# Kernel tuning notes

Hardware: AMD Instinct MI355X
Metric: run time of the kernel (lower is better)

## Reference

```python
import jax, jax.numpy as jnp
import numpy as np

EPS = 1e-9
N_HEAD = 16


def clamp_c(c):
    return jnp.clip(c, 1e-4, 1.0)


def _heads(x, H):
    B, T, C = x.shape
    return x.reshape(B, T, H, C // H)


def mobius_add(x, y, c_clamped, H):
    # per-head Mobius addition; c_clamped: (H,)
    B, T, C = x.shape
    cr = c_clamped.reshape(1, 1, H, 1)
    xr, yr = _heads(x, H), _heads(y, H)
    xn = jnp.sum(xr * xr, axis=-1, keepdims=True)
    yn = jnp.sum(yr * yr, axis=-1, keepdims=True)
    ip = jnp.sum(xr * yr, axis=-1, keepdims=True)
    num = (1 + 2 * cr * ip + cr * yn) * xr + (1 - cr * xn) * yr
    den = 1 + 2 * cr * ip + cr ** 2 * xn * yn
    return (num / (den + EPS)).reshape(B, T, C)


def expmap(x, v, c, H):
    # exponential map of tangent vector v at point x (per-head curvature)
    B, T, C = x.shape
    cc = clamp_c(c)
    cr = cc.reshape(1, 1, H, 1)
    xr, vr = _heads(x, H), _heads(v, H)
    sf = 2.0 / (1 + cr * jnp.sum(xr * xr, axis=-1, keepdims=True) + EPS)  # scaling factor
    vns = jnp.sum(vr * vr, axis=-1, keepdims=True)
    vn = jnp.sqrt(vns + EPS)
    tanh_arg = jnp.abs(cr * sf * vns / 2)
    coeff = (1.0 / (jnp.sqrt(jnp.abs(cr) + EPS) + EPS)) * jnp.tanh(jnp.sqrt(tanh_arg + EPS))
    second = (coeff * vr / (vn + EPS)).reshape(B, T, C)
    return mobius_add(x, second, cc, H)


def layernorm(x, g):
    m = jnp.mean(x, axis=-1, keepdims=True)
    v = jnp.mean((x - m) ** 2, axis=-1, keepdims=True)
    return (x - m) * jax.lax.rsqrt(v + 1e-5) * g


def attention(x, w_qkv, w_proj, H):
    B, T, C = x.shape
    hs = C // H
    q, k, v = jnp.split(x @ w_qkv.T, 3, axis=-1)
    q = q.reshape(B, T, H, hs).transpose(0, 2, 1, 3)
    k = k.reshape(B, T, H, hs).transpose(0, 2, 1, 3)
    v = v.reshape(B, T, H, hs).transpose(0, 2, 1, 3)
    att = jnp.einsum('bhqd,bhkd->bhqk', q, k) * (float(hs) ** -0.5)
    mask = jnp.tril(jnp.ones((T, T), dtype=bool))
    att = jnp.where(mask, att, -jnp.inf)
    att = jax.nn.softmax(att, axis=-1)
    y = jnp.einsum('bhqk,bhkd->bhqd', att, v)
    y = y.transpose(0, 2, 1, 3).reshape(B, T, C)
    return y @ w_proj.T


def setup_inputs() -> dict:
    key = jax.random.key(0)
    ks = jax.random.split(key, 9)
    B, T, C = 2, 2048, 1024
    s = 0.02
    return {
        'x': jax.random.normal(ks[0], (B, T, C), jnp.float32) * s,
        'ln1_g': jnp.ones((C,), jnp.float32),
        'w_qkv': jax.random.normal(ks[1], (3 * C, C), jnp.float32) * s,
        'w_attn_proj': jax.random.normal(ks[2], (C, C), jnp.float32) * s,
        'c_attn': jax.random.uniform(ks[3], (N_HEAD,), jnp.float32, 0.1, 0.9),
        'ln2_g': jnp.ones((C,), jnp.float32),
        'w_fc': jax.random.normal(ks[4], (4 * C, C), jnp.float32) * s,
        'w_mlp_proj': jax.random.normal(ks[5], (C, 4 * C), jnp.float32) * s,
        'c_mlp': jax.random.uniform(ks[6], (N_HEAD,), jnp.float32, 0.1, 0.9),
    }


def reference(x, ln1_g, w_qkv, w_attn_proj, c_attn, ln2_g, w_fc, w_mlp_proj, c_mlp):
    H = N_HEAD
    a = attention(layernorm(x, ln1_g), w_qkv, w_attn_proj, H)
    x = expmap(x, a, c_attn, H)  # hyperbolic residual (attn)
    h = jax.nn.gelu(layernorm(x, ln2_g) @ w_fc.T, approximate=False) @ w_mlp_proj.T
    x = expmap(x, h, c_mlp, H)   # hyperbolic residual (mlp)
    return x
```

## Files before the change

kernel.cpp:

```cpp
#include <hip/hip_runtime.h>
#include <hip/hip_bf16.h>

typedef __attribute__((ext_vector_type(8))) short bf16x8;
typedef __attribute__((ext_vector_type(4))) float f32x4;

typedef const __attribute__((address_space(1))) void gv_t;
typedef __attribute__((address_space(3))) void lv_t;
#define GLL16(g, l) __builtin_amdgcn_global_load_lds((gv_t*)(g), (lv_t*)(l), 16, 0, 0)

#define WAITV4()  asm volatile("s_waitcnt vmcnt(4)" ::: "memory")
#define WAITV0()  asm volatile("s_waitcnt vmcnt(0)" ::: "memory")
#define WAITL0()  asm volatile("s_waitcnt lgkmcnt(0)" ::: "memory")
#define SCHEDB()  __builtin_amdgcn_sched_barrier(0)
#define BARRAW()  __builtin_amdgcn_s_barrier()

__device__ __forceinline__ short f2bf(float f) {
    __hip_bfloat16 h = __float2bfloat16(f);
    return *reinterpret_cast<short*>(&h);
}

__device__ __forceinline__ float wred(float v) {
    #pragma unroll
    for (int m = 1; m < 64; m <<= 1) v += __shfl_xor(v, m);
    return v;
}

__global__ __launch_bounds__(256) void cvt_kernel(const float* __restrict__ in,
                                                  short* __restrict__ out, int n4) {
    int i = blockIdx.x * 256 + threadIdx.x;
    if (i < n4) {
        float4 v = ((const float4*)in)[i];
        short4 o;
        o.x = f2bf(v.x); o.y = f2bf(v.y); o.z = f2bf(v.z); o.w = f2bf(v.w);
        ((short4*)out)[i] = o;
    }
}

__global__ __launch_bounds__(256) void ln_kernel(const float* __restrict__ x,
                                                 const float* __restrict__ g,
                                                 short* __restrict__ y) {
    const int row = blockIdx.x, tid = threadIdx.x;
    const float4 v = ((const float4*)(x + (size_t)row * 1024))[tid];
    float s = v.x + v.y + v.z + v.w;
    float s2 = v.x * v.x + v.y * v.y + v.z * v.z + v.w * v.w;
    #pragma unroll
    for (int m = 1; m < 64; m <<= 1) { s += __shfl_xor(s, m); s2 += __shfl_xor(s2, m); }
    __shared__ float rs[4], rs2[4];
    if ((tid & 63) == 0) { rs[tid >> 6] = s; rs2[tid >> 6] = s2; }
    __syncthreads();
    s = rs[0] + rs[1] + rs[2] + rs[3];
    s2 = rs2[0] + rs2[1] + rs2[2] + rs2[3];
    const float mean = s * (1.0f / 1024.0f);
    const float var = s2 * (1.0f / 1024.0f) - mean * mean;
    const float r = rsqrtf(var + 1e-5f);
    const float4 gg = ((const float4*)g)[tid];
    short4 o;
    o.x = f2bf((v.x - mean) * r * gg.x);
    o.y = f2bf((v.y - mean) * r * gg.y);
    o.z = f2bf((v.z - mean) * r * gg.z);
    o.w = f2bf((v.w - mean) * r * gg.w);
    ((short4*)y)[(size_t)row * 256 + tid] = o;
}

template <int EPI>
__global__ __launch_bounds__(256, 3) void gemm_bt(const short* __restrict__ A,
                                                  const short* __restrict__ Bw,
                                                  int M, int N, int LDK, int KL,
                                                  void* __restrict__ o0,
                                                  void* __restrict__ o1,
                                                  void* __restrict__ o2) {
    __shared__ __align__(16) short As[3][128 * 32];
    __shared__ __align__(16) short Bs[3][128 * 32];
    const int tid = threadIdx.x;
    const int wid = tid >> 6, lane = tid & 63;
    const int wm = wid >> 1, wn = wid & 1;
    const int col = lane & 15, grp = lane >> 4;
    const int m0 = blockIdx.x * 128, n0 = blockIdx.y * 128;
    const int z = blockIdx.z;
    f32x4 acc[4][4] = {};
    const short* ga = A + (size_t)m0 * LDK + (size_t)z * KL;
    const short* gb = Bw + (size_t)n0 * LDK + (size_t)z * KL;

#define GSTAGE(b_, t_) do {                                                     \
        const int k0_ = (t_) * 32;                                              \
        _Pragma("unroll")                                                       \
        for (int c = 0; c < 2; ++c) {                                           \
            const int row = wid * 32 + c * 16 + (lane >> 2);                    \
            const int slot = (lane & 3) ^ ((row >> 1) & 3);                     \
            GLL16(ga + (size_t)row * LDK + k0_ + slot * 8,                      \
                  (char*)&As[b_][0] + (wid * 32 + c * 16) * 64);                \
            GLL16(gb + (size_t)row * LDK + k0_ + slot * 8,                      \
                  (char*)&Bs[b_][0] + (wid * 32 + c * 16) * 64);                \
        }                                                                       \
    } while (0)

    const int NT = KL >> 5;
    GSTAGE(0, 0);
    GSTAGE(1, 1);
    WAITV4(); SCHEDB();
    BARRAW();
    for (int t = 0; t < NT; ++t) {
        const int cur = t % 3;
        if (t + 2 < NT) GSTAGE((t + 2) % 3, t + 2);
        const char* At = (const char*)&As[cur][0];
        const char* Bt = (const char*)&Bs[cur][0];
        bf16x8 af[4], bf[4];
        #pragma unroll
        for (int i = 0; i < 4; ++i) {
            const int rowA = wm * 64 + i * 16 + col;
            const int rowB = wn * 64 + i * 16 + col;
            af[i] = *(const bf16x8*)(At + rowA * 64 + ((grp ^ ((rowA >> 1) & 3)) << 4));
            bf[i] = *(const bf16x8*)(Bt + rowB * 64 + ((grp ^ ((rowB >> 1) & 3)) << 4));
        }
        #pragma unroll
        for (int mi = 0; mi < 4; ++mi)
            #pragma unroll
            for (int ni = 0; ni < 4; ++ni)
                acc[mi][ni] = __builtin_amdgcn_mfma_f32_16x16x32_bf16(af[mi], bf[ni], acc[mi][ni], 0, 0, 0);
        if (t + 1 < NT) {
            WAITL0();
            if (t + 2 < NT) { WAITV4(); } else { WAITV0(); }
            SCHEDB();
            BARRAW();
        }
    }
#undef GSTAGE
    #pragma unroll
    for (int mi = 0; mi < 4; ++mi) {
        #pragma unroll
        for (int ni = 0; ni < 4; ++ni) {
            #pragma unroll
            for (int i = 0; i < 4; ++i) {
                const int m = m0 + wm * 64 + mi * 16 + grp * 4 + i;
                const int n = n0 + wn * 64 + ni * 16 + col;
                const float v = acc[mi][ni][i];
                if (EPI == 0) {
                    const int b = m >> 11, t = m & 2047;
                    const int which = n >> 10, nn = n & 1023;
                    const int h = nn >> 6, d = nn & 63;
                    const size_t bh = (size_t)(b * 16 + h);
                    if (which == 0)
                        ((short*)o0)[(bh * 2048 + t) * 64 + d] = f2bf(v * 0.125f);
                    else if (which == 1)
                        ((short*)o1)[(bh * 2048 + t) * 64 + d] = f2bf(v);
                    else
                        ((short*)o2)[(bh * 64 + d) * 2048 + t] = f2bf(v);
                } else if (EPI == 1) {
                    float* dst = (z == 0) ? (float*)o0 : (float*)o1;
                    dst[(size_t)m * N + n] = v;
                } else {
                    const float gl = 0.5f * v * (1.0f + erff(v * 0.70710678118654752f));
                    ((short*)o0)[(size_t)m * N + n] = f2bf(gl);
                }
            }
        }
    }
}

__global__ __launch_bounds__(256, 3) void attn_kernel(const short* __restrict__ Q,
                                                      const short* __restrict__ Kg,
                                                      const short* __restrict__ VT,
                                                      short* __restrict__ Y) {
    __shared__ __align__(16) short Ks[2][4096];
    __shared__ __align__(16) short Vs[2][4096];
    __shared__ __align__(16) short Plds[4][16 * 72];
    const int j = 31 - blockIdx.x;
    const int bh = blockIdx.y;
    const int tid = threadIdx.x, wid = tid >> 6, lane = tid & 63;
    const int ql = lane & 15, g = lane >> 4;
    const int r8 = lane >> 3, s8 = lane & 7;
    const int q0s = j * 64 + wid * 16;
    const int lt = j;
    const short* Qb = Q + (size_t)bh * 2048 * 64;
    const short* Kb = Kg + (size_t)bh * 2048 * 64;
    const short* Vb = VT + (size_t)bh * 64 * 2048;
    short* Pw = &Plds[wid][0];

    bf16x8 qf0 = *(const bf16x8*)&Qb[(size_t)(q0s + ql) * 64 + 8 * g];
    bf16x8 qf1 = *(const bf16x8*)&Qb[(size_t)(q0s + ql) * 64 + 32 + 8 * g];
    f32x4 o[4] = {};
    float m = -1e30f, lsum = 0.0f;

#define STAGE(b_, kt_) do {                                                      \
        const int kbase_ = (kt_) * 64;                                           \
        _Pragma("unroll")                                                        \
        for (int c = 0; c < 2; ++c) {                                            \
            const int row = c * 32 + wid * 8 + r8;                               \
            const int slot = s8 ^ (row & 7);                                     \
            GLL16(Kb + (size_t)(kbase_ + row) * 64 + slot * 8,                   \
                  (char*)&Ks[b_][0] + c * 4096 + wid * 1024);                    \
            GLL16(Vb + (size_t)row * 2048 + kbase_ + slot * 8,                   \
                  (char*)&Vs[b_][0] + c * 4096 + wid * 1024);                    \
        }                                                                        \
    } while (0)

    STAGE(0, 0);
    __syncthreads();
    int buf = 0;
    for (int kt = 0; kt <= lt; ++kt) {
        if (kt < lt) STAGE(buf ^ 1, kt + 1);
        const int kbase = kt * 64;
        const short* Kt = &Ks[buf][0];
        const short* Vt = &Vs[buf][0];
        bf16x8 kf[4][2];
        #pragma unroll
        for (int kb = 0; kb < 4; ++kb) {
            const int row = 16 * kb + ql;
            const int x = row & 7;
            kf[kb][0] = *(const bf16x8*)((const char*)Kt + row * 128 + ((g ^ x) << 4));
            kf[kb][1] = *(const bf16x8*)((const char*)Kt + row * 128 + (((4 + g) ^ x) << 4));
        }
        f32x4 s[4];
        #pragma unroll
        for (int kb = 0; kb < 4; ++kb) {
            f32x4 z = {0.f, 0.f, 0.f, 0.f};
            z = __builtin_amdgcn_mfma_f32_16x16x32_bf16(kf[kb][0], qf0, z, 0, 0, 0);
            z = __builtin_amdgcn_mfma_f32_16x16x32_bf16(kf[kb][1], qf1, z, 0, 0, 0);
            s[kb] = z;
        }
        if (kbase + 63 > q0s) {
            #pragma unroll
            for (int kb = 0; kb < 4; ++kb)
                #pragma unroll
                for (int r = 0; r < 4; ++r)
                    if (kbase + 16 * kb + 4 * g + r > q0s + ql) s[kb][r] = -1e30f;
        }
        float t0 = fmaxf(fmaxf(s[0][0], s[0][1]), fmaxf(s[0][2], s[0][3]));
        float t1 = fmaxf(fmaxf(s[1][0], s[1][1]), fmaxf(s[1][2], s[1][3]));
        float t2 = fmaxf(fmaxf(s[2][0], s[2][1]), fmaxf(s[2][2], s[2][3]));
        float t3 = fmaxf(fmaxf(s[3][0], s[3][1]), fmaxf(s[3][2], s[3][3]));
        float tmax = fmaxf(fmaxf(t0, t1), fmaxf(t2, t3));
        tmax = fmaxf(tmax, __shfl_xor(tmax, 16));
        tmax = fmaxf(tmax, __shfl_xor(tmax, 32));
        const float mnew = fmaxf(m, tmax);
        const float sc = __expf(m - mnew);
        m = mnew;
        float rsum = 0.0f;
        #pragma unroll
        for (int kb = 0; kb < 4; ++kb) {
            const float e0 = __expf(s[kb][0] - mnew);
            const float e1 = __expf(s[kb][1] - mnew);
            const float e2 = __expf(s[kb][2] - mnew);
            const float e3 = __expf(s[kb][3] - mnew);
            rsum += (e0 + e1) + (e2 + e3);
            short4 pk;
            pk.x = f2bf(e0); pk.y = f2bf(e1); pk.z = f2bf(e2); pk.w = f2bf(e3);
            *(short4*)&Pw[ql * 72 + 16 * kb + 4 * g] = pk;
        }
        rsum += __shfl_xor(rsum, 16);
        rsum += __shfl_xor(rsum, 32);
        lsum = lsum * sc + rsum;
        #pragma unroll
        for (int nf = 0; nf < 4; ++nf)
            #pragma unroll
            for (int r = 0; r < 4; ++r) o[nf][r] *= sc;
        const bf16x8 pb0 = *(const bf16x8*)&Pw[ql * 72 + 8 * g];
        const bf16x8 pb1 = *(const bf16x8*)&Pw[ql * 72 + 32 + 8 * g];
        #pragma unroll
        for (int nf = 0; nf < 4; ++nf) {
            const int row = 16 * nf + ql;
            const int x = row & 7;
            bf16x8 v0 = *(const bf16x8*)((const char*)Vt + row * 128 + ((g ^ x) << 4));
            bf16x8 v1 = *(const bf16x8*)((const char*)Vt + row * 128 + (((4 + g) ^ x) << 4));
            o[nf] = __builtin_amdgcn_mfma_f32_16x16x32_bf16(v0, pb0, o[nf], 0, 0, 0);
            o[nf] = __builtin_amdgcn_mfma_f32_16x16x32_bf16(v1, pb1, o[nf], 0, 0, 0);
        }
        __syncthreads();
        buf ^= 1;
    }
#undef STAGE
    const int b = bh >> 4, h = bh & 15;
    const float inv = 1.0f / lsum;
    const size_t rowoff = ((size_t)b * 2048 + q0s + ql) * 1024 + h * 64;
    #pragma unroll
    for (int nf = 0; nf < 4; ++nf) {
        short4 w;
        w.x = f2bf(o[nf][0] * inv);
        w.y = f2bf(o[nf][1] * inv);
        w.z = f2bf(o[nf][2] * inv);
        w.w = f2bf(o[nf][3] * inv);
        *(short4*)&Y[rowoff + 16 * nf + 4 * g] = w;
    }
}

__global__ __launch_bounds__(256) void expmap_kernel(const float* __restrict__ x,
                                                     const float* __restrict__ va,
                                                     const float* __restrict__ vb,
                                                     const float* __restrict__ carr,
                                                     float* __restrict__ out) {
    const int blk = blockIdx.x;
    const int row = blk >> 2;
    const int head = (blk & 3) * 4 + (threadIdx.x >> 6);
    const int lane = threadIdx.x & 63;
    const size_t idx = (size_t)row * 1024 + head * 64 + lane;
    float c = carr[head];
    c = fminf(fmaxf(c, 1e-4f), 1.0f);
    const float xe = x[idx], ve = va[idx] + vb[idx];
    const float xn = wred(xe * xe);
    const float vns = wred(ve * ve);
    const float vn = sqrtf(vns + 1e-9f);
    const float sf = 2.0f / (1.0f + c * xn + 1e-9f);
    const float targ = fabsf(0.5f * c * sf * vns);
    const float coeff = (1.0f / (sqrtf(c + 1e-9f) + 1e-9f)) * tanhf(sqrtf(targ + 1e-9f));
    const float ye = coeff * ve / (vn + 1e-9f);
    const float yn = wred(ye * ye);
    const float ip = wred(xe * ye);
    const float num = (1.0f + 2.0f * c * ip + c * yn) * xe + (1.0f - c * xn) * ye;
    const float den = 1.0f + 2.0f * c * ip + c * c * xn * yn;
    out[idx] = num / (den + 1e-9f);
}

extern "C" void kernel_launch(void* const* d_in, const int* in_sizes, int n_in,
                              void* d_out, int out_size, void* d_ws, size_t ws_size,
                              hipStream_t stream) {
    (void)in_sizes; (void)n_in; (void)out_size; (void)ws_size;
    const float* x      = (const float*)d_in[0];
    const float* ln1_g  = (const float*)d_in[1];
    const float* w_qkv  = (const float*)d_in[2];
    const float* w_proj = (const float*)d_in[3];
    const float* c_attn = (const float*)d_in[4];
    const float* ln2_g  = (const float*)d_in[5];
    const float* w_fc   = (const float*)d_in[6];
    const float* w_mlp  = (const float*)d_in[7];
    const float* c_mlp  = (const float*)d_in[8];
    float* out = (float*)d_out;
    char* ws = (char*)d_ws;
    const size_t MB = 1024 * 1024;

    short* wqkv_bf  = (short*)(ws + 0 * MB);
    short* wproj_bf = (short*)(ws + 6 * MB);
    short* wfc_bf   = (short*)(ws + 8 * MB);
    short* wmlp_bf  = (short*)(ws + 16 * MB);
    short* y_bf     = (short*)(ws + 24 * MB);
    short* q_bf     = (short*)(ws + 32 * MB);
    short* k_bf     = (short*)(ws + 40 * MB);
    short* vT_bf    = (short*)(ws + 48 * MB);
    short* att_bf   = (short*)(ws + 56 * MB);
    float* a0       = (float*)(ws + 64 * MB);
    float* a1       = (float*)(ws + 80 * MB);
    float* x1       = (float*)(ws + 40 * MB);
    short* g_bf     = (short*)(ws + 56 * MB);
    float* h0       = (float*)(ws + 0 * MB);
    float* h1       = (float*)(ws + 24 * MB);

    cvt_kernel<<<3072, 256, 0, stream>>>(w_qkv, wqkv_bf, 3072 * 1024 / 4);
    cvt_kernel<<<1024, 256, 0, stream>>>(w_proj, wproj_bf, 1024 * 1024 / 4);
    cvt_kernel<<<4096, 256, 0, stream>>>(w_fc, wfc_bf, 4096 * 1024 / 4);
    cvt_kernel<<<4096, 256, 0, stream>>>(w_mlp, wmlp_bf, 1024 * 4096 / 4);

    ln_kernel<<<4096, 256, 0, stream>>>(x, ln1_g, y_bf);
    gemm_bt<0><<<dim3(32, 24, 1), 256, 0, stream>>>(y_bf, wqkv_bf, 4096, 3072, 1024, 1024,
                                                    q_bf, k_bf, vT_bf);
    attn_kernel<<<dim3(32, 32), 256, 0, stream>>>(q_bf, k_bf, vT_bf, att_bf);
    gemm_bt<1><<<dim3(32, 8, 2), 256, 0, stream>>>(att_bf, wproj_bf, 4096, 1024, 1024, 512,
                                                   a0, a1, nullptr);
    expmap_kernel<<<16384, 256, 0, stream>>>(x, a0, a1, c_attn, x1);
    ln_kernel<<<4096, 256, 0, stream>>>(x1, ln2_g, y_bf);
    gemm_bt<2><<<dim3(32, 32, 1), 256, 0, stream>>>(y_bf, wfc_bf, 4096, 4096, 1024, 1024,
                                                    g_bf, nullptr, nullptr);
    gemm_bt<1><<<dim3(32, 8, 2), 256, 0, stream>>>(g_bf, wmlp_bf, 4096, 1024, 4096, 2048,
                                                   h0, h1, nullptr);
    expmap_kernel<<<16384, 256, 0, stream>>>(x1, h0, h1, c_mlp, out);
}
```

Before: 316.4 us.

## Use 64-wide K tiles with double buffering and XCD-aware tile swizzle in GEMM

The bf16 GEMM now stages 64-element K slices in two LDS buffers instead of 32-element slices in three. Each thread loads all fragments into registers, then hits a barrier and immediately reuses the freed buffer for the stage two ahead, which halves the number of loop iterations and barriers. Block indices are also remapped so each XCD covers a contiguous band of M and N tiles, aiming for better L2 reuse. The costs are more registers and LDS per block, with occupancy dropping from 3 to 2 blocks per SIMD. The swizzle also assumes particular grid shapes: gridDim.y must be divisible by 4 and gridDim.x must be 32.

Result: faster. 299.4 us (-5.4%).

```diff
diff --git a/kernel.cpp b/kernel.cpp
--- a/kernel.cpp
+++ b/kernel.cpp
@@ -8,7 +8,7 @@
 typedef __attribute__((address_space(3))) void lv_t;
 #define GLL16(g, l) __builtin_amdgcn_global_load_lds((gv_t*)(g), (lv_t*)(l), 16, 0, 0)
 
-#define WAITV4()  asm volatile("s_waitcnt vmcnt(4)" ::: "memory")
+#define WAITV8()  asm volatile("s_waitcnt vmcnt(8)" ::: "memory")
 #define WAITV0()  asm volatile("s_waitcnt vmcnt(0)" ::: "memory")
 #define WAITL0()  asm volatile("s_waitcnt lgkmcnt(0)" ::: "memory")
 #define SCHEDB()  __builtin_amdgcn_sched_barrier(0)
@@ -63,66 +63,78 @@
 }
 
 template <int EPI>
-__global__ __launch_bounds__(256, 3) void gemm_bt(const short* __restrict__ A,
+__global__ __launch_bounds__(256, 2) void gemm_bt(const short* __restrict__ A,
                                                   const short* __restrict__ Bw,
                                                   int M, int N, int LDK, int KL,
                                                   void* __restrict__ o0,
                                                   void* __restrict__ o1,
                                                   void* __restrict__ o2) {
-    __shared__ __align__(16) short As[3][128 * 32];
-    __shared__ __align__(16) short Bs[3][128 * 32];
+    __shared__ __align__(16) short As[2][128 * 64];
+    __shared__ __align__(16) short Bs[2][128 * 64];
     const int tid = threadIdx.x;
     const int wid = tid >> 6, lane = tid & 63;
     const int wm = wid >> 1, wn = wid & 1;
     const int col = lane & 15, grp = lane >> 4;
-    const int m0 = blockIdx.x * 128, n0 = blockIdx.y * 128;
+    const int r8 = lane >> 3, s8 = lane & 7;
+    const int orig = blockIdx.x + (int)gridDim.x * blockIdx.y;
+    const int xcd = orig & 7, idx = orig >> 3;
+    const int NC = gridDim.y >> 2;
+    const int mt = ((xcd >> 2) << 4) + (idx & 15);
+    const int nt = (xcd & 3) * NC + (idx >> 4);
+    const int m0 = mt * 128, n0 = nt * 128;
     const int z = blockIdx.z;
     f32x4 acc[4][4] = {};
     const short* ga = A + (size_t)m0 * LDK + (size_t)z * KL;
     const short* gb = Bw + (size_t)n0 * LDK + (size_t)z * KL;
 
 #define GSTAGE(b_, t_) do {                                                     \
-        const int k0_ = (t_) * 32;                                              \
+        const int k0_ = (t_) * 64;                                              \
         _Pragma("unroll")                                                       \
-        for (int c = 0; c < 2; ++c) {                                           \
-            const int row = wid * 32 + c * 16 + (lane >> 2);                    \
-            const int slot = (lane & 3) ^ ((row >> 1) & 3);                     \
+        for (int c = 0; c < 4; ++c) {                                           \
+            const int row = c * 32 + wid * 8 + r8;                              \
+            const int slot = s8 ^ (row & 7);                                    \
             GLL16(ga + (size_t)row * LDK + k0_ + slot * 8,                      \
-                  (char*)&As[b_][0] + (wid * 32 + c * 16) * 64);                \
+                  (char*)&As[b_][0] + c * 4096 + wid * 1024);                   \
             GLL16(gb + (size_t)row * LDK + k0_ + slot * 8,                      \
-                  (char*)&Bs[b_][0] + (wid * 32 + c * 16) * 64);                \
+                  (char*)&Bs[b_][0] + c * 4096 + wid * 1024);                   \
         }                                                                       \
     } while (0)
 
-    const int NT = KL >> 5;
+    const int NT = KL >> 6;
     GSTAGE(0, 0);
-    GSTAGE(1, 1);
-    WAITV4(); SCHEDB();
+    if (NT > 1) { GSTAGE(1, 1); WAITV8(); } else { WAITV0(); }
+    SCHEDB();
     BARRAW();
+    int cur = 0;
     for (int t = 0; t < NT; ++t) {
-        const int cur = t % 3;
-        if (t + 2 < NT) GSTAGE((t + 2) % 3, t + 2);
         const char* At = (const char*)&As[cur][0];
         const char* Bt = (const char*)&Bs[cur][0];
-        bf16x8 af[4], bf[4];
-        #pragma unroll
-        for (int i = 0; i < 4; ++i) {
-            const int rowA = wm * 64 + i * 16 + col;
-            const int rowB = wn * 64 + i * 16 + col;
-            af[i] = *(const bf16x8*)(At + rowA * 64 + ((grp ^ ((rowA >> 1) & 3)) << 4));
-            bf[i] = *(const bf16x8*)(Bt + rowB * 64 + ((grp ^ ((rowB >> 1) & 3)) << 4));
-        }
-        #pragma unroll
-        for (int mi = 0; mi < 4; ++mi)
-            #pragma unroll
-            for (int ni = 0; ni < 4; ++ni)
-                acc[mi][ni] = __builtin_amdgcn_mfma_f32_16x16x32_bf16(af[mi], bf[ni], acc[mi][ni], 0, 0, 0);
+        bf16x8 af[2][4], bfr[2][4];
+        #pragma unroll
+        for (int s = 0; s < 2; ++s)
+            #pragma unroll
+            for (int i = 0; i < 4; ++i) {
+                const int rowA = wm * 64 + i * 16 + col;
+                const int rowB = wn * 64 + i * 16 + col;
+                af[s][i]  = *(const bf16x8*)(At + rowA * 128 + (((s * 4 + grp) ^ (rowA & 7)) << 4));
+                bfr[s][i] = *(const bf16x8*)(Bt + rowB * 128 + (((s * 4 + grp) ^ (rowB & 7)) << 4));
+            }
+        WAITL0(); SCHEDB();
+        BARRAW();
+        if (t + 2 < NT) GSTAGE(cur, t + 2);
+        #pragma unroll
+        for (int s = 0; s < 2; ++s)
+            #pragma unroll
+            for (int mi = 0; mi < 4; ++mi)
+                #pragma unroll
+                for (int ni = 0; ni < 4; ++ni)
+                    acc[mi][ni] = __builtin_amdgcn_mfma_f32_16x16x32_bf16(af[s][mi], bfr[s][ni], acc[mi][ni], 0, 0, 0);
         if (t + 1 < NT) {
-            WAITL0();
-            if (t + 2 < NT) { WAITV4(); } else { WAITV0(); }
+            if (t + 2 < NT) { WAITV8(); } else { WAITV0(); }
             SCHEDB();
             BARRAW();
         }
+        cur ^= 1;
     }
 #undef GSTAGE
     #pragma unroll
```
